# Kernel tuning notes

Hardware: AMD Instinct MI355X
Metric: run time of the kernel (lower is better)

## Reference

```python
import jax, jax.numpy as jnp
import numpy as np

B, N, E = 16, 2048, 32768   # graphs per batch, nodes per graph, edges per graph
V, D, R, L = 50000, 256, 8, 2  # vocab, embed dim, num relations, gnn layers


def setup_inputs() -> dict:
    key = jax.random.key(0)
    ks = jax.random.split(key, 7)
    nodes = jax.random.randint(ks[0], (B, N), 0, V)
    edges = jax.random.randint(ks[1], (B, 2, E), 0, N)
    types = jax.random.randint(ks[2], (B, E), 0, R)
    emb = jax.random.normal(ks[3], (V, D), jnp.float32) * 0.02
    W = jax.random.normal(ks[4], (L, R, D, D), jnp.float32) * (1.0 / np.sqrt(D))
    W_root = jax.random.normal(ks[5], (L, D, D), jnp.float32) * (1.0 / np.sqrt(D))
    b = jnp.zeros((L, D), jnp.float32)
    return dict(nodes=nodes, edges=edges, types=types, emb=emb, W=W, W_root=W_root, b=b)


def _rgcn_layer(x, src, dst, etype, W, W_root, b):
    # x: [N,D]; src/dst/etype: [E]; W: [R,D,D]; W_root: [D,D]; b: [D]
    n = x.shape[0]
    xw = jnp.einsum('nd,rde->rne', x, W)          # per-relation transform [R,N,D]
    msgs = xw[etype, src]                          # gather per-edge messages [E,D]
    agg = jax.ops.segment_sum(msgs, dst, num_segments=n)          # scatter-add [N,D]
    deg = jax.ops.segment_sum(jnp.ones((src.shape[0],), x.dtype), dst, num_segments=n)
    return agg / jnp.maximum(deg, 1.0)[:, None] + x @ W_root + b  # mean aggr + self loop


def reference(nodes, edges, types, emb, W, W_root, b):
    x = emb[nodes]                                  # [B,N,D] per-sample embedding lookup
    src, dst = edges[:, 0], edges[:, 1]
    layer = jax.vmap(_rgcn_layer, in_axes=(0, 0, 0, 0, None, None, None))
    for l in range(L):
        x = layer(x, src, dst, types, W[l], W_root[l], b[l])
        if l < L - 1:
            x = jax.nn.relu(x)  # dropout is identity at inference
    return x
```

## Files before the change

### kernel.cpp

```cpp
#include <hip/hip_runtime.h>

#define BB 16
#define NN 2048
#define EE 32768
#define DD 256
#define RR 8
#define LL 2
#define BUCKETS (RR * NN)
#define TM 64

typedef unsigned short u16;
typedef __attribute__((__ext_vector_type__(8))) __bf16 bfx8;
typedef __attribute__((__ext_vector_type__(16))) float fx16;

__device__ __forceinline__ float blo(unsigned u){ union{unsigned x;float f;}c; c.x=u<<16; return c.f; }
__device__ __forceinline__ float bhi(unsigned u){ union{unsigned x;float f;}c; c.x=u&0xffff0000u; return c.f; }
__device__ __forceinline__ u16 f2bf(float f){ union{float f;unsigned u;}x; x.f=f;
    return (u16)((x.u + 0x7FFFu + ((x.u>>16)&1u))>>16); }
__device__ __forceinline__ unsigned pk2(float a, float b){
    return (unsigned)f2bf(a) | ((unsigned)f2bf(b)<<16); }
__device__ __forceinline__ void acc8(float* a, uint4 p0, uint4 p1) {
    a[0]+=blo(p0.x); a[1]+=bhi(p0.x); a[2]+=blo(p0.y); a[3]+=bhi(p0.y);
    a[4]+=blo(p0.z); a[5]+=bhi(p0.z); a[6]+=blo(p0.w); a[7]+=bhi(p0.w);
    a[8]+=blo(p1.x); a[9]+=bhi(p1.x); a[10]+=blo(p1.y); a[11]+=bhi(p1.y);
    a[12]+=blo(p1.z); a[13]+=bhi(p1.z); a[14]+=blo(p1.w); a[15]+=bhi(p1.w);
}

__global__ __launch_bounds__(256) void prep0(const float* __restrict__ W,
                                             const float* __restrict__ Wroot,
                                             u16* __restrict__ Wf,
                                             int* __restrict__ counts, int bc)
{
    int t = threadIdx.x;
    if (blockIdx.x < 8 * LL * 9) {
        __shared__ float tl[32][257];
        int kt = blockIdx.x & 7, ls = blockIdx.x >> 3;
        int l = ls / 9, seg = ls - l * 9;
        const float* src = (seg < 8) ? W + (size_t)(l * RR + seg) * DD * DD
                                     : Wroot + (size_t)l * DD * DD;
        for (int k8 = 0; k8 < 32; ++k8)
            tl[k8][t] = src[(size_t)(kt * 32 + k8) * DD + t];
        __syncthreads();
        #pragma unroll
        for (int i = 0; i < 4; ++i) {
            int o = i * 256 + t;
            int fl = o & 63, ks2 = (o >> 6) & 1, nt8 = o >> 7;
            int n = nt8 * 32 + (fl & 31);
            int kb = ks2 * 16 + (fl >> 5) * 8;
            unsigned d0 = pk2(tl[kb + 0][n], tl[kb + 1][n]);
            unsigned d1 = pk2(tl[kb + 2][n], tl[kb + 3][n]);
            unsigned d2 = pk2(tl[kb + 4][n], tl[kb + 5][n]);
            unsigned d3 = pk2(tl[kb + 6][n], tl[kb + 7][n]);
            *(uint4*)(Wf + (((size_t)ls * 8 + kt) * 1024 + o) * 8) =
                make_uint4(d0, d1, d2, d3);
        }
    } else {
        int idx = (blockIdx.x - 8 * LL * 9) * 256 + t;
        int tot = bc * BUCKETS / 4;
        if (idx < tot) ((int4*)counts)[idx] = make_int4(0, 0, 0, 0);
    }
}

__global__ __launch_bounds__(256) void prep1(const int* __restrict__ nodes,
                                             const float* __restrict__ emb,
                                             u16* __restrict__ x0,
                                             const int* __restrict__ edges,
                                             const int* __restrict__ types,
                                             int* __restrict__ counts,
                                             int b0, int bc)
{
    int ng = bc * 512;
    if ((int)blockIdx.x < ng) {
        int t = blockIdx.x * 256 + threadIdx.x;
        int lane = t & 63;
        int row = t >> 6;
        int bb = row / NN;
        int n  = row - bb * NN;
        int v  = nodes[(size_t)(b0 + bb) * NN + n];
        float4 val = *((const float4*)(emb + (size_t)v * DD) + lane);
        ushort4 o;
        o.x = f2bf(val.x); o.y = f2bf(val.y); o.z = f2bf(val.z); o.w = f2bf(val.w);
        *((ushort4*)(x0 + (size_t)row * DD) + lane) = o;
    } else {
        int t = (blockIdx.x - ng) * 256 + threadIdx.x;
        int bb = t / EE;
        int e  = t - bb * EE;
        const int* eb = edges + (size_t)(b0 + bb) * 2 * EE;
        int dst = eb[EE + e];
        int r   = types[(size_t)(b0 + bb) * EE + e];
        atomicAdd(&counts[((size_t)bb * RR + r) * NN + dst], 1);
    }
}

__global__ __launch_bounds__(256) void scan2_k(const int* __restrict__ counts,
                                               int* __restrict__ offsets,
                                               int* __restrict__ cursor,
                                               float* __restrict__ invdeg)
{
    int bb = blockIdx.x;
    int tid = threadIdx.x;
    size_t base = (size_t)bb * BUCKETS;
    __shared__ int sums[256];

    int tot = 0;
    #pragma unroll 4
    for (int i = 0; i < 64; ++i) tot += counts[base + tid * 64 + i];
    sums[tid] = tot;
    __syncthreads();
    for (int off = 1; off < 256; off <<= 1) {
        int v = (tid >= off) ? sums[tid - off] : 0;
        __syncthreads();
        sums[tid] += v;
        __syncthreads();
    }
    int run = sums[tid] - tot;
    for (int i = 0; i < 64; ++i) {
        size_t idx = base + tid * 64 + i;
        offsets[idx] = run;
        cursor[idx]  = run;
        run += counts[idx];
    }
    #pragma unroll
    for (int i = 0; i < 8; ++i) {
        int n = tid * 8 + i;
        int d = 0;
        #pragma unroll
        for (int r = 0; r < RR; ++r)
            d += counts[base + (size_t)r * NN + n];
        invdeg[(size_t)bb * NN + n] = 1.0f / fmaxf((float)d, 1.0f);
    }
}

__global__ __launch_bounds__(256) void permute_k(const int* __restrict__ edges,
                                                 const int* __restrict__ types,
                                                 int* __restrict__ cursor,
                                                 int* __restrict__ edgeSrc,
                                                 int b0, int bc)
{
    int t = blockIdx.x * 256 + threadIdx.x;
    int bb = t / EE;
    int e  = t - bb * EE;
    const int* eb = edges + (size_t)(b0 + bb) * 2 * EE;
    int src = eb[e];
    int dst = eb[EE + e];
    int r   = types[(size_t)(b0 + bb) * EE + e];
    int pos = atomicAdd(&cursor[((size_t)bb * RR + r) * NN + dst], 1);
    edgeSrc[(size_t)bb * EE + pos] = src;
}

__device__ __forceinline__ void build_seg(int seg, u16* A,
                                          const int* sStart, const int* sCnt,
                                          const int* es, const u16* xb, int m0,
                                          int gid, int j16, int ks0, int lh2)
{
    #pragma unroll
    for (int rr = 0; rr < 2; ++rr) {
        int row = gid * 2 + rr;
        int mt = row >> 5, m31 = row & 31;
        int flw = m31 + 32 * lh2;
        unsigned w0, w1, w2, w3, w4, w5, w6, w7;
        if (seg < 8) {
            float a[16];
            #pragma unroll
            for (int e = 0; e < 16; ++e) a[e] = 0.0f;
            int start = sStart[seg * TM + row];
            int cnt   = sCnt[seg * TM + row];
            const int* ep = es + start;
            int jj = 0;
            for (; jj + 2 <= cnt; jj += 2) {
                int s0 = ep[jj], s1 = ep[jj + 1];
                const u16* xr0 = xb + (size_t)s0 * DD;
                const u16* xr1 = xb + (size_t)s1 * DD;
                uint4 p0 = *(const uint4*)(xr0 + j16 * 8);
                uint4 p1 = *(const uint4*)(xr0 + 128 + j16 * 8);
                uint4 q0 = *(const uint4*)(xr1 + j16 * 8);
                uint4 q1 = *(const uint4*)(xr1 + 128 + j16 * 8);
                acc8(a, p0, p1);
                acc8(a, q0, q1);
            }
            if (jj < cnt) {
                const u16* xr0 = xb + (size_t)ep[jj] * DD;
                uint4 p0 = *(const uint4*)(xr0 + j16 * 8);
                uint4 p1 = *(const uint4*)(xr0 + 128 + j16 * 8);
                acc8(a, p0, p1);
            }
            w0 = pk2(a[0], a[1]);   w1 = pk2(a[2], a[3]);
            w2 = pk2(a[4], a[5]);   w3 = pk2(a[6], a[7]);
            w4 = pk2(a[8], a[9]);   w5 = pk2(a[10], a[11]);
            w6 = pk2(a[12], a[13]); w7 = pk2(a[14], a[15]);
        } else {
            const u16* xr = xb + (size_t)(m0 + row) * DD;
            uint4 p0 = *(const uint4*)(xr + j16 * 8);
            uint4 p1 = *(const uint4*)(xr + 128 + j16 * 8);
            w0 = p0.x; w1 = p0.y; w2 = p0.z; w3 = p0.w;
            w4 = p1.x; w5 = p1.y; w6 = p1.z; w7 = p1.w;
        }
        int c0 = ((mt * 16 + ks0) * 64 + ((flw + ks0) & 63)) * 8;
        int c1 = ((mt * 16 + ks0 + 8) * 64 + ((flw + ks0 + 8) & 63)) * 8;
        *(uint4*)&A[c0] = make_uint4(w0, w1, w2, w3);
        *(uint4*)&A[c1] = make_uint4(w4, w5, w6, w7);
    }
}

template <int WRITE_BF16>
__global__ __launch_bounds__(512, 4) void rgcn_fused(
    const int* __restrict__ offsets, const int* __restrict__ counts,
    const int* __restrict__ edgeSrc, const u16* __restrict__ xin,
    const u16* __restrict__ Wf,
    const float* __restrict__ bias, const float* __restrict__ invdeg,
    float* __restrict__ outF, u16* __restrict__ outH, int relu, int bc)
{
    __shared__ __align__(16) u16 Af[2][16384];
    __shared__ float sInv[TM];
    __shared__ int sStart[8 * TM], sCnt[8 * TM];

    int t = threadIdx.x;
    int fl = t & 63;
    int wid = t >> 6;
    int bid = blockIdx.x;
    int bb, mt0;
    if (bc == 16) {
        bb  = (bid & 7) * 2 + ((bid >> 3) & 1);
        mt0 = bid >> 4;
    } else {
        bb  = bid >> 5;
        mt0 = bid & 31;
    }
    int m0 = mt0 * TM;

    {
        int r = t >> 6, row = t & 63;
        int g = ((bb * RR + r) * NN) + m0 + row;
        sStart[t] = offsets[g];
        sCnt[t]   = counts[g];
    }
    if (t < TM) sInv[t] = invdeg[(size_t)bb * NN + m0 + t];

    const u16* xb = xin + (size_t)bb * NN * DD;
    const int* es = edgeSrc + (size_t)bb * EE;

    int gid = t >> 4;
    int j16 = t & 15;
    int ks0 = j16 >> 1;
    int lh2 = j16 & 1;
    int lh = fl >> 5;

    fx16 acc[2];
    #pragma unroll
    for (int mt = 0; mt < 2; ++mt)
        #pragma unroll
        for (int e = 0; e < 16; ++e) acc[mt][e] = 0.0f;

    __syncthreads();
    build_seg(0, Af[0], sStart, sCnt, es, xb, m0, gid, j16, ks0, lh2);
    __syncthreads();

    for (int seg = 0; seg < 9; ++seg) {
        if (seg < 8)
            build_seg(seg + 1, Af[(seg + 1) & 1], sStart, sCnt, es, xb, m0,
                      gid, j16, ks0, lh2);

        if (seg == 8) {
            #pragma unroll
            for (int mt = 0; mt < 2; ++mt)
                #pragma unroll
                for (int r = 0; r < 16; ++r) {
                    int rl = mt * 32 + (r & 3) + 8 * (r >> 2) + 4 * lh;
                    acc[mt][r] *= sInv[rl];
                }
        }

        const u16* Wseg = Wf + (size_t)seg * 65536;
        const u16* A = Af[seg & 1];
        #pragma unroll 2
        for (int kt = 0; kt < 8; ++kt) {
            bfx8 bfr[2], af[2][2];
            #pragma unroll
            for (int ks2 = 0; ks2 < 2; ++ks2) {
                int ksA = kt * 2 + ks2;
                bfr[ks2] = *(const bfx8*)(Wseg + (size_t)kt * 8192 + wid * 1024
                                          + ks2 * 512 + fl * 8);
                af[0][ks2] = *(const bfx8*)&A[((0  + ksA) * 64 + ((fl + ksA) & 63)) * 8];
                af[1][ks2] = *(const bfx8*)&A[((16 + ksA) * 64 + ((fl + ksA) & 63)) * 8];
            }
            #pragma unroll
            for (int ks2 = 0; ks2 < 2; ++ks2) {
                acc[0] = __builtin_amdgcn_mfma_f32_32x32x16_bf16(af[0][ks2], bfr[ks2], acc[0], 0, 0, 0);
                acc[1] = __builtin_amdgcn_mfma_f32_32x32x16_bf16(af[1][ks2], bfr[ks2], acc[1], 0, 0, 0);
            }
        }
        __syncthreads();
    }

    int col = wid * 32 + (fl & 31);
    float bv = bias[col];
    #pragma unroll
    for (int mt = 0; mt < 2; ++mt)
        #pragma unroll
        for (int r = 0; r < 16; ++r) {
            int row = m0 + mt * 32 + (r & 3) + 8 * (r >> 2) + 4 * lh;
            float v = acc[mt][r] + bv;
            if (relu) v = fmaxf(v, 0.0f);
            if (WRITE_BF16)
                outH[((size_t)bb * NN + row) * DD + col] = f2bf(v);
            else
                outF[((size_t)bb * NN + row) * DD + col] = v;
        }
}

extern "C" void kernel_launch(void* const* d_in, const int* in_sizes, int n_in,
                              void* d_out, int out_size, void* d_ws, size_t ws_size,
                              hipStream_t stream)
{
    const int*   nodes = (const int*)d_in[0];
    const int*   edges = (const int*)d_in[1];
    const int*   types = (const int*)d_in[2];
    const float* emb   = (const float*)d_in[3];
    const float* W     = (const float*)d_in[4];
    const float* Wroot = (const float*)d_in[5];
    const float* bias  = (const float*)d_in[6];
    float* out = (float*)d_out;

    const size_t wfElems = (size_t)LL * 9 * 8 * 1024 * 8;
    const size_t fixedBytes = wfElems * sizeof(u16);
    const size_t perBatchBytes =
        2 * (size_t)NN * DD * sizeof(u16) + (size_t)NN * sizeof(float) +
        (3 * (size_t)BUCKETS + EE) * sizeof(int);
    int BC = (int)((ws_size - fixedBytes) / perBatchBytes);
    if (BC > BB) BC = BB;
    if (BC < 1) BC = 1;

    u16* Wf      = (u16*)d_ws;
    u16* x0      = Wf + wfElems;
    u16* x1      = x0 + (size_t)BC * NN * DD;
    float* invdeg = (float*)(x1 + (size_t)BC * NN * DD);
    int* counts  = (int*)(invdeg + (size_t)BC * NN);
    int* offsets = counts + (size_t)BC * BUCKETS;
    int* cursor  = offsets + (size_t)BC * BUCKETS;
    int* edgeSrc = cursor + (size_t)BC * BUCKETS;

    for (int b0 = 0; b0 < BB; b0 += BC) {
        int bc = BB - b0 < BC ? BB - b0 : BC;

        int zeroBlocks = (bc * BUCKETS / 4 + 255) / 256;
        prep0<<<8 * LL * 9 + zeroBlocks, 256, 0, stream>>>(W, Wroot, Wf, counts, bc);
        prep1<<<bc * 640, 256, 0, stream>>>(nodes, emb, x0, edges, types, counts, b0, bc);
        scan2_k<<<bc, 256, 0, stream>>>(counts, offsets, cursor, invdeg);
        permute_k<<<bc * 128, 256, 0, stream>>>(edges, types, cursor, edgeSrc, b0, bc);

        for (int l = 0; l < LL; ++l) {
            const u16* xin = (l == 0) ? x0 : x1;
            const u16* Wfl = Wf + (size_t)l * 9 * 65536;
            if (l == 0)
                rgcn_fused<1><<<bc * 32, 512, 0, stream>>>(offsets, counts, edgeSrc,
                    xin, Wfl, bias + (size_t)l * DD, invdeg, nullptr, x1, 1, bc);
            else
                rgcn_fused<0><<<bc * 32, 512, 0, stream>>>(offsets, counts, edgeSrc,
                    xin, Wfl, bias + (size_t)l * DD, invdeg,
                    out + (size_t)b0 * NN * DD, nullptr, 0, bc);
        }
    }
}
```

Before: 301.0 us.

## Single-buffer LDS A tile with wave-per-row gather to raise occupancy

Drops the double-buffered A tile in shared memory, so segment building no longer overlaps the MFMA loop, and raises the launch-bounds occupancy hint from 4 to 6. The gather is restructured so each wave handles 8 rows and each lane loads 4 bf16 values (8 bytes) per edge, instead of 16 lanes per row loading 32 bytes each. The aim is fewer registers and less LDS per block, allowing more resident blocks to hide gather latency. The cost is losing the explicit build/compute overlap, an extra barrier per segment, and narrower, more numerous gather loads.

```diff
diff --git a/kernel.cpp b/kernel.cpp
--- a/kernel.cpp
+++ b/kernel.cpp
@@ -12,6 +12,7 @@
 typedef unsigned short u16;
 typedef __attribute__((__ext_vector_type__(8))) __bf16 bfx8;
 typedef __attribute__((__ext_vector_type__(16))) float fx16;
+typedef __attribute__((__ext_vector_type__(2))) float f32x2;
 
 __device__ __forceinline__ float blo(unsigned u){ union{unsigned x;float f;}c; c.x=u<<16; return c.f; }
 __device__ __forceinline__ float bhi(unsigned u){ union{unsigned x;float f;}c; c.x=u&0xffff0000u; return c.f; }
@@ -19,12 +20,6 @@
     return (u16)((x.u + 0x7FFFu + ((x.u>>16)&1u))>>16); }
 __device__ __forceinline__ unsigned pk2(float a, float b){
     return (unsigned)f2bf(a) | ((unsigned)f2bf(b)<<16); }
-__device__ __forceinline__ void acc8(float* a, uint4 p0, uint4 p1) {
-    a[0]+=blo(p0.x); a[1]+=bhi(p0.x); a[2]+=blo(p0.y); a[3]+=bhi(p0.y);
-    a[4]+=blo(p0.z); a[5]+=bhi(p0.z); a[6]+=blo(p0.w); a[7]+=bhi(p0.w);
-    a[8]+=blo(p1.x); a[9]+=bhi(p1.x); a[10]+=blo(p1.y); a[11]+=bhi(p1.y);
-    a[12]+=blo(p1.z); a[13]+=bhi(p1.z); a[14]+=blo(p1.w); a[15]+=bhi(p1.w);
-}
 
 __global__ __launch_bounds__(256) void prep0(const float* __restrict__ W,
                                              const float* __restrict__ Wroot,
@@ -148,74 +143,21 @@
     edgeSrc[(size_t)bb * EE + pos] = src;
 }
 
-__device__ __forceinline__ void build_seg(int seg, u16* A,
-                                          const int* sStart, const int* sCnt,
-                                          const int* es, const u16* xb, int m0,
-                                          int gid, int j16, int ks0, int lh2)
-{
-    #pragma unroll
-    for (int rr = 0; rr < 2; ++rr) {
-        int row = gid * 2 + rr;
-        int mt = row >> 5, m31 = row & 31;
-        int flw = m31 + 32 * lh2;
-        unsigned w0, w1, w2, w3, w4, w5, w6, w7;
-        if (seg < 8) {
-            float a[16];
-            #pragma unroll
-            for (int e = 0; e < 16; ++e) a[e] = 0.0f;
-            int start = sStart[seg * TM + row];
-            int cnt   = sCnt[seg * TM + row];
-            const int* ep = es + start;
-            int jj = 0;
-            for (; jj + 2 <= cnt; jj += 2) {
-                int s0 = ep[jj], s1 = ep[jj + 1];
-                const u16* xr0 = xb + (size_t)s0 * DD;
-                const u16* xr1 = xb + (size_t)s1 * DD;
-                uint4 p0 = *(const uint4*)(xr0 + j16 * 8);
-                uint4 p1 = *(const uint4*)(xr0 + 128 + j16 * 8);
-                uint4 q0 = *(const uint4*)(xr1 + j16 * 8);
-                uint4 q1 = *(const uint4*)(xr1 + 128 + j16 * 8);
-                acc8(a, p0, p1);
-                acc8(a, q0, q1);
-            }
-            if (jj < cnt) {
-                const u16* xr0 = xb + (size_t)ep[jj] * DD;
-                uint4 p0 = *(const uint4*)(xr0 + j16 * 8);
-                uint4 p1 = *(const uint4*)(xr0 + 128 + j16 * 8);
-                acc8(a, p0, p1);
-            }
-            w0 = pk2(a[0], a[1]);   w1 = pk2(a[2], a[3]);
-            w2 = pk2(a[4], a[5]);   w3 = pk2(a[6], a[7]);
-            w4 = pk2(a[8], a[9]);   w5 = pk2(a[10], a[11]);
-            w6 = pk2(a[12], a[13]); w7 = pk2(a[14], a[15]);
-        } else {
-            const u16* xr = xb + (size_t)(m0 + row) * DD;
-            uint4 p0 = *(const uint4*)(xr + j16 * 8);
-            uint4 p1 = *(const uint4*)(xr + 128 + j16 * 8);
-            w0 = p0.x; w1 = p0.y; w2 = p0.z; w3 = p0.w;
-            w4 = p1.x; w5 = p1.y; w6 = p1.z; w7 = p1.w;
-        }
-        int c0 = ((mt * 16 + ks0) * 64 + ((flw + ks0) & 63)) * 8;
-        int c1 = ((mt * 16 + ks0 + 8) * 64 + ((flw + ks0 + 8) & 63)) * 8;
-        *(uint4*)&A[c0] = make_uint4(w0, w1, w2, w3);
-        *(uint4*)&A[c1] = make_uint4(w4, w5, w6, w7);
-    }
-}
-
 template <int WRITE_BF16>
-__global__ __launch_bounds__(512, 4) void rgcn_fused(
+__global__ __launch_bounds__(512, 6) void rgcn_fused(
     const int* __restrict__ offsets, const int* __restrict__ counts,
     const int* __restrict__ edgeSrc, const u16* __restrict__ xin,
     const u16* __restrict__ Wf,
     const float* __restrict__ bias, const float* __restrict__ invdeg,
     float* __restrict__ outF, u16* __restrict__ outH, int relu, int bc)
 {
-    __shared__ __align__(16) u16 Af[2][16384];
+    __shared__ __align__(16) u16 Af[16384];
     __shared__ float sInv[TM];
     __shared__ int sStart[8 * TM], sCnt[8 * TM];
 
     int t = threadIdx.x;
     int fl = t & 63;
+    int lane = fl;
     int wid = t >> 6;
     int bid = blockIdx.x;
     int bb, mt0;
@@ -239,10 +181,9 @@
     const u16* xb = xin + (size_t)bb * NN * DD;
     const int* es = edgeSrc + (size_t)bb * EE;
 
-    int gid = t >> 4;
-    int j16 = t & 15;
-    int ks0 = j16 >> 1;
-    int lh2 = j16 & 1;
+    int ksA_w = lane >> 2;
+    int lh_w  = (lane >> 1) & 1;
+    int half_w = lane & 1;
     int lh = fl >> 5;
 
     fx16 acc[2];
@@ -252,13 +193,44 @@
         for (int e = 0; e < 16; ++e) acc[mt][e] = 0.0f;
 
     __syncthreads();
-    build_seg(0, Af[0], sStart, sCnt, es, xb, m0, gid, j16, ks0, lh2);
-    __syncthreads();
 
     for (int seg = 0; seg < 9; ++seg) {
-        if (seg < 8)
-            build_seg(seg + 1, Af[(seg + 1) & 1], sStart, sCnt, es, xb, m0,
-                      gid, j16, ks0, lh2);
+        #pragma unroll 2
+        for (int rr = 0; rr < 8; ++rr) {
+            int row = wid * 8 + rr;
+            unsigned w0, w1;
+            if (seg < 8) {
+                f32x2 a01 = {0.f, 0.f}, a23 = {0.f, 0.f};
+                int start = sStart[seg * TM + row];
+                int cnt   = sCnt[seg * TM + row];
+                const int* ep = es + start;
+                int j = 0;
+                for (; j + 2 <= cnt; j += 2) {
+                    int s0 = ep[j], s1 = ep[j + 1];
+                    uint2 p = *(const uint2*)(xb + (size_t)s0 * DD + lane * 4);
+                    uint2 q = *(const uint2*)(xb + (size_t)s1 * DD + lane * 4);
+                    f32x2 p01 = {blo(p.x), bhi(p.x)}, p23 = {blo(p.y), bhi(p.y)};
+                    f32x2 q01 = {blo(q.x), bhi(q.x)}, q23 = {blo(q.y), bhi(q.y)};
+                    a01 += p01; a23 += p23;
+                    a01 += q01; a23 += q23;
+                }
+                if (j < cnt) {
+                    uint2 p = *(const uint2*)(xb + (size_t)ep[j] * DD + lane * 4);
+                    f32x2 p01 = {blo(p.x), bhi(p.x)}, p23 = {blo(p.y), bhi(p.y)};
+                    a01 += p01; a23 += p23;
+                }
+                w0 = pk2(a01.x, a01.y);
+                w1 = pk2(a23.x, a23.y);
+            } else {
+                uint2 p = *(const uint2*)(xb + (size_t)(m0 + row) * DD + lane * 4);
+                w0 = p.x; w1 = p.y;
+            }
+            int mt = row >> 5, m31 = row & 31;
+            int flw = m31 + 32 * lh_w;
+            int off = ((mt * 16 + ksA_w) * 64 + ((flw + ksA_w) & 63)) * 8 + half_w * 4;
+            *(uint2*)&Af[off] = make_uint2(w0, w1);
+        }
+        __syncthreads();
 
         if (seg == 8) {
             #pragma unroll
@@ -271,7 +243,6 @@
         }
 
         const u16* Wseg = Wf + (size_t)seg * 65536;
-        const u16* A = Af[seg & 1];
         #pragma unroll 2
         for (int kt = 0; kt < 8; ++kt) {
             bfx8 bfr[2], af[2][2];
@@ -280,8 +251,8 @@
                 int ksA = kt * 2 + ks2;
                 bfr[ks2] = *(const bfx8*)(Wseg + (size_t)kt * 8192 + wid * 1024
                                           + ks2 * 512 + fl * 8);
-                af[0][ks2] = *(const bfx8*)&A[((0  + ksA) * 64 + ((fl + ksA) & 63)) * 8];
-                af[1][ks2] = *(const bfx8*)&A[((16 + ksA) * 64 + ((fl + ksA) & 63)) * 8];
+                af[0][ks2] = *(const bfx8*)&Af[((0  + ksA) * 64 + ((fl + ksA) & 63)) * 8];
+                af[1][ks2] = *(const bfx8*)&Af[((16 + ksA) * 64 + ((fl + ksA) & 63)) * 8];
             }
             #pragma unroll
             for (int ks2 = 0; ks2 < 2; ++ks2) {
```

Result: slower. 328.3 us (+9.1%).
